# Performance work log

Hardware: AMD Instinct MI355X
Metric: run time of the kernel (lower is better)

Reference implementation:

```python
import jax, jax.numpy as jnp
import numpy as np

EPS = 1e-7
B, C, H, W = 8, 128, 256, 256
HEADS, P = 8, 8
P2 = P * P  # 64
KSIZE = 3


def setup_inputs() -> dict:
    key = jax.random.key(0)
    ks = jax.random.split(key, 9)
    s = 0.05
    x = jax.random.normal(ks[0], (B, C, H, W), jnp.float32)
    Wq = jax.random.normal(ks[1], (P2 * HEADS, P2), jnp.float32) * s
    bq = jax.random.normal(ks[2], (P2 * HEADS,), jnp.float32) * s
    Wk = jax.random.normal(ks[3], (P2 * HEADS, P2), jnp.float32) * s
    bk = jax.random.normal(ks[4], (P2 * HEADS,), jnp.float32) * s
    Wv = jax.random.normal(ks[5], (C, C), jnp.float32) * s  # 1x1 conv squeezed
    bv = jax.random.normal(ks[6], (C,), jnp.float32) * s
    Wp = jax.random.normal(ks[7], (C, 1, KSIZE, KSIZE), jnp.float32) * s  # depthwise
    bp = jax.random.normal(ks[8], (C,), jnp.float32) * s
    return {"x": x, "Wq": Wq, "bq": bq, "Wk": Wk, "bk": bk,
            "Wv": Wv, "bv": bv, "Wp": Wp, "bp": bp}


def _linear_attn(q, k, xv):
    # q, k: [B, heads, C, P2]; xv: [B, heads, C, d2]
    l1, d1 = q.shape[-2], q.shape[-1]
    l2, d2 = xv.shape[-2], xv.shape[-1]
    if l1 * d1 * l2 + l1 * l2 * d2 <= d2 * l2 * d1 + d2 * d1 * l1:
        qk = jnp.einsum('bhcp,bhdp->bhcd', q, k)          # q @ k^T : [B,h,C,C]
        qk = qk / (qk.sum(axis=-1, keepdims=True) + EPS)
        return jnp.einsum('bhcd,bhde->bhce', qk, xv)
    else:
        kx = jnp.einsum('bhcp,bhcd->bhpd', k, xv)          # k^T @ x : [B,h,P2,d2]
        out = jnp.einsum('bhcp,bhpd->bhcd', q, kx)         # q @ (k^T @ x)
        denom = jnp.einsum('bhcp,bhp->bhc', q, k.sum(axis=2)) + EPS  # q @ rowsum(k^T)
        return out / denom[..., None]


def reference(x, Wq, bq, Wk, bk, Wv, bv, Wp, bp):
    Bs, Cs, Hs, Ws = x.shape
    # AdaptiveAvgPool2d(P) with divisible dims == block mean
    pooled = x.reshape(Bs, Cs, P, Hs // P, P, Ws // P).mean(axis=(3, 5))
    pooled = pooled.reshape(Bs, Cs, P2)
    q = jax.nn.relu(pooled @ Wq.T + bq).reshape(Bs, Cs, HEADS, P2).transpose(0, 2, 1, 3)
    k = jax.nn.relu(pooled @ Wk.T + bk).reshape(Bs, Cs, HEADS, P2).transpose(0, 2, 1, 3)
    # 1x1 conv (v)
    v = jnp.einsum('bchw,oc->bohw', x, Wv) + bv[None, :, None, None]
    d2 = (Hs * Ws) // HEADS  # divisible by construction -> no replicate pad
    xv = v.reshape(Bs, Cs, HEADS, d2).transpose(0, 2, 1, 3)
    attn = _linear_attn(q, k, xv)                           # [B,h,C,d2]
    out = attn.transpose(0, 2, 1, 3).reshape(Bs, Cs, Hs, Ws)
    # depthwise 3x3 proj, padding 1
    out = jax.lax.conv_general_dilated(
        out, Wp, window_strides=(1, 1), padding=[(1, 1), (1, 1)],
        dimension_numbers=('NCHW', 'OIHW', 'NCHW'), feature_group_count=Cs)
    return out + bp[None, :, None, None]
```

## Files before the change

kernel.cpp:

```cpp
#include <hip/hip_runtime.h>
#include <hip/hip_bf16.h>

#define HW 65536
#define CCH 128

typedef __attribute__((ext_vector_type(8))) short short8;
typedef __attribute__((ext_vector_type(4))) float f32x4;
typedef __attribute__((ext_vector_type(8))) unsigned short u16x8;

__device__ __forceinline__ void gload_lds16(const void* g, void* l) {
    __builtin_amdgcn_global_load_lds((const __attribute__((address_space(1))) void*)g,
                                     (__attribute__((address_space(3))) void*)l, 16, 0, 0);
}
__device__ __forceinline__ unsigned short f2bf(float f) {
    union { float f; unsigned int i; } u; u.f = f;
    unsigned int r = u.i + 0x7fffu + ((u.i >> 16) & 1u);
    return (unsigned short)(r >> 16);
}
__device__ __forceinline__ float bf2f(unsigned short h) {
    union { unsigned int i; float f; } u; u.i = ((unsigned int)h) << 16; return u.f;
}
__device__ __forceinline__ unsigned int cvt_pk_bf16(float lo, float hi) {
    unsigned int r;
    asm("v_cvt_pk_bf16_f32 %0, %1, %2" : "=v"(r) : "v"(lo), "v"(hi));
    return r;
}
__device__ __forceinline__ void lds_barrier() {
    asm volatile("s_waitcnt lgkmcnt(0)" ::: "memory");
    __builtin_amdgcn_s_barrier();
    __builtin_amdgcn_sched_barrier(0);
}

__global__ __launch_bounds__(256) void pool_kernel(const float* __restrict__ x,
                                                   float* __restrict__ pooled) {
    int bc = blockIdx.x;
    const float* base = x + (size_t)bc * HW;
    int t = threadIdx.x;
    int w = t >> 6, l = t & 63;
    for (int it = 0; it < 2; ++it) {
        int py = w + it * 4;
        const float* rp = base + py * 32 * 256 + l * 4;
        f32x4 s0 = {0.f, 0.f, 0.f, 0.f};
        f32x4 s1 = {0.f, 0.f, 0.f, 0.f};
        #pragma unroll
        for (int r = 0; r < 32; r += 2) {
            s0 += *(const f32x4*)(rp + r * 256);
            s1 += *(const f32x4*)(rp + (r + 1) * 256);
        }
        f32x4 sv = s0 + s1;
        float acc = sv[0] + sv[1] + sv[2] + sv[3];
        acc += __shfl_down(acc, 4, 8);
        acc += __shfl_down(acc, 2, 8);
        acc += __shfl_down(acc, 1, 8);
        if ((l & 7) == 0)
            pooled[(size_t)bc * 64 + py * 8 + (l >> 3)] = acc * (1.0f / 1024.0f);
    }
}

__global__ __launch_bounds__(256) void qkam_kernel(
        const float* __restrict__ pooled,
        const float* __restrict__ Wq, const float* __restrict__ bq,
        const float* __restrict__ Wk, const float* __restrict__ bk,
        const float* __restrict__ bv,
        unsigned short* __restrict__ Ahi, unsigned short* __restrict__ Alo,
        float* __restrict__ beta) {
    int bid = blockIdx.x;
    int bh = bid >> 2;
    int cg = bid & 3;
    int b = bh >> 3, h = bh & 7;
    int t = threadIdx.x;
    __shared__ float ps[128 * 64];
    __shared__ float Wqs[64 * 64];
    __shared__ float Wks[64 * 64];
    __shared__ float ks[128 * 68];
    __shared__ float qs[32 * 68];
    __shared__ float bvs[128];

    for (int i = t; i < 2048; i += 256) {
        int c = i >> 4, p4 = (i & 15) * 4;
        *(f32x4*)&ps[c * 64 + p4] = *(const f32x4*)(pooled + (size_t)(b * CCH + c) * 64 + p4);
    }
    for (int i = t; i < 1024; i += 256) {
        int r = i >> 4, p4 = (i & 15) * 4;
        *(f32x4*)&Wqs[r * 64 + p4] = *(const f32x4*)(Wq + (size_t)(h * 64 + r) * 64 + p4);
        *(f32x4*)&Wks[r * 64 + p4] = *(const f32x4*)(Wk + (size_t)(h * 64 + r) * 64 + p4);
    }
    if (t < 128) bvs[t] = bv[t];
    __syncthreads();

    {
        int p = t & 63, g = t >> 6;
        f32x4 wr[16];
        #pragma unroll
        for (int j = 0; j < 16; ++j) wr[j] = *(const f32x4*)&Wks[p * 64 + j * 4];
        float bkv = bk[h * 64 + p];
        for (int dd = 0; dd < 32; ++dd) {
            int d = g * 32 + dd;
            float acc = bkv;
            #pragma unroll
            for (int j = 0; j < 16; ++j) {
                f32x4 pv = *(const f32x4*)&ps[d * 64 + j * 4];
                acc += pv[0] * wr[j][0] + pv[1] * wr[j][1] + pv[2] * wr[j][2] + pv[3] * wr[j][3];
            }
            ks[d * 68 + p] = fmaxf(acc, 0.f);
        }
        #pragma unroll
        for (int j = 0; j < 16; ++j) wr[j] = *(const f32x4*)&Wqs[p * 64 + j * 4];
        float bqv = bq[h * 64 + p];
        for (int dd = 0; dd < 8; ++dd) {
            int cl = g * 8 + dd;
            int c = cg * 32 + cl;
            float acc = bqv;
            #pragma unroll
            for (int j = 0; j < 16; ++j) {
                f32x4 pv = *(const f32x4*)&ps[c * 64 + j * 4];
                acc += pv[0] * wr[j][0] + pv[1] * wr[j][1] + pv[2] * wr[j][2] + pv[3] * wr[j][3];
            }
            qs[cl * 68 + p] = fmaxf(acc, 0.f);
        }
    }
    __syncthreads();

    {
        int cl = t >> 3, dc = t & 7;
        int c = cg * 32 + cl;
        int d0 = dc * 16;
        f32x4 qr[16];
        #pragma unroll
        for (int ch = 0; ch < 16; ++ch) qr[ch] = *(const f32x4*)&qs[cl * 68 + ch * 4];
        float a[16];
        #pragma unroll
        for (int jr = 0; jr < 16; ++jr) {
            int j = (jr + dc * 2) & 15;
            int d = d0 + j;
            float acc = 0.f;
            #pragma unroll
            for (int ch = 0; ch < 16; ++ch) {
                f32x4 kr = *(const f32x4*)&ks[d * 68 + ch * 4];
                acc += qr[ch][0] * kr[0] + qr[ch][1] * kr[1] + qr[ch][2] * kr[2] + qr[ch][3] * kr[3];
            }
            a[j] = acc;
        }
        float s = 0.f;
        #pragma unroll
        for (int j = 0; j < 16; ++j) s += a[j];
        s += __shfl_xor(s, 1);
        s += __shfl_xor(s, 2);
        s += __shfl_xor(s, 4);
        float inv = 1.0f / (s + 1e-7f);
        float bpart = 0.f;
        union { unsigned short u[16]; uint4 v[2]; } ph, pl;
        #pragma unroll
        for (int j = 0; j < 16; ++j) {
            float an = a[j] * inv;
            bpart += an * bvs[d0 + j];
            unsigned short hi = f2bf(an);
            ph.u[j] = hi;
            pl.u[j] = f2bf(an - bf2f(hi));
        }
        bpart += __shfl_xor(bpart, 1);
        bpart += __shfl_xor(bpart, 2);
        bpart += __shfl_xor(bpart, 4);
        if (dc == 0) beta[bh * 128 + c] = bpart;
        size_t ao = (size_t)bh * 16384 + c * 128 + d0;
        *(uint4*)(Ahi + ao) = ph.v[0];
        *(uint4*)(Ahi + ao + 8) = ph.v[1];
        *(uint4*)(Alo + ao) = pl.v[0];
        *(uint4*)(Alo + ao + 8) = pl.v[1];
    }
}

__global__ __launch_bounds__(256) void am2_kernel(
        const unsigned short* __restrict__ Ahi, const unsigned short* __restrict__ Alo,
        const float* __restrict__ Wv, unsigned short* __restrict__ Mo) {
    int bid = blockIdx.x;
    int bh = bid >> 1;
    int eg = bid & 1;
    int tid = threadIdx.x;
    __shared__ __align__(16) char Wt[65536];
    for (int i = tid; i < 4096; i += 256) {
        int d = i >> 5, e4 = (i & 31) * 4;
        f32x4 v = *(const f32x4*)(Wv + (size_t)d * 128 + e4);
        #pragma unroll
        for (int j = 0; j < 4; ++j) {
            int e = e4 + j;
            unsigned short hi = f2bf(v[j]);
            unsigned short lo = f2bf(v[j] - bf2f(hi));
            int o = (e * 256 + d * 2) ^ ((e & 7) << 4);
            *(unsigned short*)(Wt + o) = hi;
            *(unsigned short*)(Wt + 32768 + o) = lo;
        }
    }
    __syncthreads();
    int w = tid >> 6, l = tid & 63;
    int lc = l & 15, lk = (l >> 4) * 8;
    f32x4 acc[2][4] = {};
    const unsigned short* Ab = Ahi + (size_t)bh * 16384;
    const unsigned short* Alb = Alo + (size_t)bh * 16384;
    #pragma unroll
    for (int ksi = 0; ksi < 4; ++ksi) {
        int d = ksi * 32 + lk;
        short8 ah[2], al[2], bhv[4], blv[4];
        #pragma unroll
        for (int ci = 0; ci < 2; ++ci) {
            int c = w * 32 + ci * 16 + lc;
            ah[ci] = *(const short8*)(Ab + c * 128 + d);
            al[ci] = *(const short8*)(Alb + c * 128 + d);
        }
        #pragma unroll
        for (int ei = 0; ei < 4; ++ei) {
            int e = eg * 64 + ei * 16 + lc;
            int o = (e * 256 + d * 2) ^ ((e & 7) << 4);
            bhv[ei] = *(const short8*)(Wt + o);
            blv[ei] = *(const short8*)(Wt + 32768 + o);
        }
        #pragma unroll
        for (int ci = 0; ci < 2; ++ci)
            #pragma unroll
            for (int ei = 0; ei < 4; ++ei) {
                acc[ci][ei] = __builtin_amdgcn_mfma_f32_16x16x32_bf16(ah[ci], bhv[ei], acc[ci][ei], 0, 0, 0);
                acc[ci][ei] = __builtin_amdgcn_mfma_f32_16x16x32_bf16(ah[ci], blv[ei], acc[ci][ei], 0, 0, 0);
                acc[ci][ei] = __builtin_amdgcn_mfma_f32_16x16x32_bf16(al[ci], bhv[ei], acc[ci][ei], 0, 0, 0);
            }
    }
    unsigned short* Mb = Mo + (size_t)bh * 16384;
    #pragma unroll
    for (int ci = 0; ci < 2; ++ci)
        #pragma unroll
        for (int ei = 0; ei < 4; ++ei)
            #pragma unroll
            for (int r = 0; r < 4; ++r) {
                int c = w * 32 + ci * 16 + (l >> 4) * 4 + r;
                int e = eg * 64 + ei * 16 + lc;
                Mb[c * 128 + e] = f2bf(acc[ci][ei][r]);
            }
}

__global__ __launch_bounds__(512, 4) void attn_kernel(
        const float* __restrict__ x,
        const __hip_bfloat16* __restrict__ Mbf,
        const float* __restrict__ beta,
        __hip_bfloat16* __restrict__ attn) {
    int bid = blockIdx.x;
    int bh = bid >> 3;
    int chunk = bid & 7;
    int b = bh >> 3, h = bh & 7;
    int s0g = h * 8192 + chunk * 1024;
    int tid = threadIdx.x;
    int w = tid >> 6, l = tid & 63;

    __shared__ __align__(16) char sm[81920];
    char* ts0 = sm + 32768;
    char* ost = sm + 65536;

    const char* Mg = (const char*)(Mbf + (size_t)bh * 16384);
    #pragma unroll
    for (int i = 0; i < 4; ++i) {
        int o = i * 8192 + tid * 16;
        int osw = o ^ (((o >> 8) & 15) << 4);
        gload_lds16(Mg + osw, sm + o);
    }

    int e0u = (tid >> 4) * 2;
    int s4u = (tid & 15) * 4;
    const float* xb = x + (size_t)b * CCH * HW + s0g;

    f32x4 rg[4];
    #define LOADT(t_) do { \
        const float* p0 = xb + (size_t)e0u * HW + (t_) * 64 + s4u; \
        rg[0] = *(const f32x4*)p0; \
        rg[1] = *(const f32x4*)(p0 + HW); \
        const float* p1 = p0 + (size_t)64 * HW; \
        rg[2] = *(const f32x4*)p1; \
        rg[3] = *(const f32x4*)(p1 + HW); \
    } while (0)
    #define WRITET(buf_) do { \
        _Pragma("unroll") \
        for (int j = 0; j < 4; ++j) { \
            int s = s4u + j; \
            int sw = (s & 15) << 4; \
            unsigned int pa = cvt_pk_bf16(rg[0][j], rg[1][j]); \
            unsigned int pb = cvt_pk_bf16(rg[2][j], rg[3][j]); \
            *(unsigned int*)((buf_) + ((s * 256 + e0u * 2) ^ sw)) = pa; \
            *(unsigned int*)((buf_) + ((s * 256 + (e0u + 64) * 2) ^ sw)) = pb; \
        } \
    } while (0)

    LOADT(0);
    WRITET(ts0);
    LOADT(1);
    __syncthreads();

    int c0w = (w >> 1) * 32;
    int s0w = (w & 1) * 32;
    short8 mf[2][4];
    #pragma unroll
    for (int ci = 0; ci < 2; ++ci)
        #pragma unroll
        for (int ksi = 0; ksi < 4; ++ksi) {
            int c = c0w + ci * 16 + (l & 15);
            int o = (c * 256 + ksi * 64 + ((l >> 4) * 16)) ^ ((c & 15) << 4);
            mf[ci][ksi] = *(const short8*)(sm + o);
        }
    const float* bet = beta + bh * 128;
    float bv0 = bet[c0w + (l & 15)];
    float bv1 = bet[c0w + 16 + (l & 15)];
    __hip_bfloat16* ab = attn + (size_t)b * CCH * HW + s0g;

    for (int t = 0; t < 16; ++t) {
        char* tsc = ts0 + (t & 1) * 16384;
        if (t < 15) WRITET(ts0 + ((t + 1) & 1) * 16384);
        if (t < 14) LOADT(t + 2);
        f32x4 acc[2][2] = {};
        #pragma unroll
        for (int ksi = 0; ksi < 4; ++ksi) {
            short8 af[2];
            #pragma unroll
            for (int si = 0; si < 2; ++si) {
                int s = s0w + si * 16 + (l & 15);
                int o = (s * 256 + ksi * 64 + ((l >> 4) * 16)) ^ ((s & 15) << 4);
                af[si] = *(const short8*)(tsc + o);
            }
            #pragma unroll
            for (int si = 0; si < 2; ++si)
                #pragma unroll
                for (int ci = 0; ci < 2; ++ci)
                    acc[si][ci] = __builtin_amdgcn_mfma_f32_16x16x32_bf16(af[si], mf[ci][ksi], acc[si][ci], 0, 0, 0);
        }
        #pragma unroll
        for (int si = 0; si < 2; ++si)
            #pragma unroll
            for (int ci = 0; ci < 2; ++ci) {
                int sb = s0w + si * 16 + (l >> 4) * 4;
                int c = c0w + ci * 16 + (l & 15);
                float bvv = ci ? bv1 : bv0;
                uint2 pk2;
                pk2.x = cvt_pk_bf16(acc[si][ci][0] + bvv, acc[si][ci][1] + bvv);
                pk2.y = cvt_pk_bf16(acc[si][ci][2] + bvv, acc[si][ci][3] + bvv);
                int o = (c * 128 + sb * 2) ^ ((c & 7) << 4);
                *(uint2*)(ost + o) = pk2;
            }
        lds_barrier();
        #pragma unroll
        for (int p = 0; p < 2; ++p) {
            int c = p * 64 + (tid >> 3);
            int kk = tid & 7;
            int o = (c * 128 + kk * 16) ^ ((c & 7) << 4);
            *(int4*)((char*)(ab + (size_t)c * HW + t * 64) + kk * 16) = *(const int4*)(ost + o);
        }
        lds_barrier();
    }
    #undef LOADT
    #undef WRITET
}

__global__ __launch_bounds__(256) void dwconv_kernel(const __hip_bfloat16* __restrict__ attn,
        const float* __restrict__ Wp, const float* __restrict__ bp,
        float* __restrict__ out) {
    int bid = blockIdx.x;
    int bc = bid >> 3;
    int ys = bid & 7;
    int y0 = ys * 32;
    int t = threadIdx.x;
    __shared__ unsigned short tile[34][264];
    const unsigned short* base = (const unsigned short*)attn + (size_t)bc * HW;
    for (int i = t; i < 34 * 32; i += 256) {
        int r = i >> 5, ck = i & 31;
        int gy = y0 + r - 1;
        u16x8 v;
        if (gy >= 0 && gy < 256) v = *(const u16x8*)(base + gy * 256 + ck * 8);
        else v = (u16x8)((unsigned short)0);
        *(u16x8*)&tile[r][ck * 8] = v;
    }
    __syncthreads();
    int c = bc & 127;
    float wv[9];
    #pragma unroll
    for (int j = 0; j < 9; ++j) wv[j] = Wp[c * 9 + j];
    float bias = bp[c];
    float* obase = out + (size_t)bc * HW;
    for (int p = 0; p < 4; ++p) {
        int orow = p * 8 + (t >> 5);
        int oc = (t & 31) * 8;
        float accv[8];
        #pragma unroll
        for (int j = 0; j < 8; ++j) accv[j] = bias;
        #pragma unroll
        for (int dy = 0; dy < 3; ++dy) {
            int tr = orow + dy;
            u16x8 m = *(const u16x8*)&tile[tr][oc];
            float f[10];
            f[0] = (oc == 0) ? 0.f : bf2f(tile[tr][oc - 1]);
            #pragma unroll
            for (int j = 0; j < 8; ++j) f[j + 1] = bf2f(m[j]);
            f[9] = (oc == 248) ? 0.f : bf2f(tile[tr][oc + 8]);
            float w0 = wv[dy * 3], w1 = wv[dy * 3 + 1], w2 = wv[dy * 3 + 2];
            #pragma unroll
            for (int j = 0; j < 8; ++j)
                accv[j] += w0 * f[j] + w1 * f[j + 1] + w2 * f[j + 2];
        }
        float* op = obase + (size_t)(y0 + orow) * 256 + oc;
        float4 o0 = {accv[0], accv[1], accv[2], accv[3]};
        float4 o1 = {accv[4], accv[5], accv[6], accv[7]};
        *(float4*)op = o0;
        *(float4*)(op + 4) = o1;
    }
}

extern "C" void kernel_launch(void* const* d_in, const int* in_sizes, int n_in,
                              void* d_out, int out_size, void* d_ws, size_t ws_size,
                              hipStream_t stream) {
    const float* x  = (const float*)d_in[0];
    const float* Wq = (const float*)d_in[1];
    const float* bq = (const float*)d_in[2];
    const float* Wk = (const float*)d_in[3];
    const float* bk = (const float*)d_in[4];
    const float* Wv = (const float*)d_in[5];
    const float* bv = (const float*)d_in[6];
    const float* Wp = (const float*)d_in[7];
    const float* bp = (const float*)d_in[8];
    float* out = (float*)d_out;
    char* ws = (char*)d_ws;

    float* pooled      = (float*)ws;
    unsigned short* Ahi = (unsigned short*)(ws + 262144);
    unsigned short* Alo = (unsigned short*)(ws + 2359296);
    unsigned short* Mo  = (unsigned short*)(ws + 4456448);
    float* betab       = (float*)(ws + 6553600);
    char* attnp        = ws + 6586368;

    pool_kernel<<<dim3(1024), dim3(256), 0, stream>>>(x, pooled);
    qkam_kernel<<<dim3(256), dim3(256), 0, stream>>>(pooled, Wq, bq, Wk, bk, bv, Ahi, Alo, betab);
    am2_kernel<<<dim3(128), dim3(256), 0, stream>>>(Ahi, Alo, Wv, Mo);
    attn_kernel<<<dim3(512), dim3(512), 0, stream>>>(x, (const __hip_bfloat16*)Mo, betab, (__hip_bfloat16*)attnp);
    dwconv_kernel<<<dim3(8192), dim3(256), 0, stream>>>((const __hip_bfloat16*)attnp, Wp, bp, out);
}
```

Baseline: 266.4 us.

## Rebalance attn kernel work over 768 blocks and shrink LDS for higher occupancy

The attention GEMM kernel now splits each (batch, head) into 12 blocks of 10–11 tiles instead of 8 blocks of 16 tiles, launching 768 blocks to fill the GPU's 256 CUs more evenly. LDS use drops from 80KB to 48KB by reusing the M staging area for the x tile double buffer once the M fragments are in registers, and launch bounds rise to 6 waves-per-EU to allow more resident blocks. The cost is an extra barrier, uneven per-block work (10 vs 11 tiles), and possibly more register pressure under the tighter launch bound.

```diff
diff --git a/kernel.cpp b/kernel.cpp
--- a/kernel.cpp
+++ b/kernel.cpp
@@ -236,38 +236,30 @@
             }
 }
 
-__global__ __launch_bounds__(512, 4) void attn_kernel(
+__global__ __launch_bounds__(512, 6) void attn_kernel(
         const float* __restrict__ x,
         const __hip_bfloat16* __restrict__ Mbf,
         const float* __restrict__ beta,
         __hip_bfloat16* __restrict__ attn) {
     int bid = blockIdx.x;
-    int bh = bid >> 3;
-    int chunk = bid & 7;
+    int bh = bid / 12;
+    int r12 = bid % 12;
     int b = bh >> 3, h = bh & 7;
-    int s0g = h * 8192 + chunk * 1024;
+    int start = (r12 < 8) ? r12 * 11 : 88 + (r12 - 8) * 10;
+    int ntile = (r12 < 8) ? 11 : 10;
     int tid = threadIdx.x;
     int w = tid >> 6, l = tid & 63;
 
-    __shared__ __align__(16) char sm[81920];
-    char* ts0 = sm + 32768;
-    char* ost = sm + 65536;
-
-    const char* Mg = (const char*)(Mbf + (size_t)bh * 16384);
-    #pragma unroll
-    for (int i = 0; i < 4; ++i) {
-        int o = i * 8192 + tid * 16;
-        int osw = o ^ (((o >> 8) & 15) << 4);
-        gload_lds16(Mg + osw, sm + o);
-    }
+    __shared__ __align__(16) char sm[49152];
+    char* ost = sm + 32768;
 
     int e0u = (tid >> 4) * 2;
     int s4u = (tid & 15) * 4;
-    const float* xb = x + (size_t)b * CCH * HW + s0g;
+    const float* xb = x + (size_t)b * CCH * HW + h * 8192;
 
     f32x4 rg[4];
-    #define LOADT(t_) do { \
-        const float* p0 = xb + (size_t)e0u * HW + (t_) * 64 + s4u; \
+    #define LOADT(T_) do { \
+        const float* p0 = xb + (size_t)e0u * HW + (T_) * 64 + s4u; \
         rg[0] = *(const f32x4*)p0; \
         rg[1] = *(const f32x4*)(p0 + HW); \
         const float* p1 = p0 + (size_t)64 * HW; \
@@ -286,9 +278,14 @@
         } \
     } while (0)
 
-    LOADT(0);
-    WRITET(ts0);
-    LOADT(1);
+    LOADT(start);
+    const char* Mg = (const char*)(Mbf + (size_t)bh * 16384);
+    #pragma unroll
+    for (int i = 0; i < 4; ++i) {
+        int o = i * 8192 + tid * 16;
+        int osw = o ^ (((o >> 8) & 15) << 4);
+        gload_lds16(Mg + osw, sm + o);
+    }
     __syncthreads();
 
     int c0w = (w >> 1) * 32;
@@ -305,12 +302,17 @@
     const float* bet = beta + bh * 128;
     float bv0 = bet[c0w + (l & 15)];
     float bv1 = bet[c0w + 16 + (l & 15)];
-    __hip_bfloat16* ab = attn + (size_t)b * CCH * HW + s0g;
-
-    for (int t = 0; t < 16; ++t) {
-        char* tsc = ts0 + (t & 1) * 16384;
-        if (t < 15) WRITET(ts0 + ((t + 1) & 1) * 16384);
-        if (t < 14) LOADT(t + 2);
+    __hip_bfloat16* ab = attn + (size_t)b * CCH * HW + h * 8192;
+    lds_barrier();
+
+    WRITET(sm);
+    LOADT(start + 1);
+    lds_barrier();
+
+    for (int t = 0; t < ntile; ++t) {
+        char* tsc = sm + (t & 1) * 16384;
+        if (t + 1 < ntile) WRITET(sm + ((t + 1) & 1) * 16384);
+        if (t + 2 < ntile) LOADT(start + t + 2);
         f32x4 acc[2][2] = {};
         #pragma unroll
         for (int ksi = 0; ksi < 4; ++ksi) {
@@ -341,12 +343,13 @@
                 *(uint2*)(ost + o) = pk2;
             }
         lds_barrier();
+        int T = start + t;
         #pragma unroll
         for (int p = 0; p < 2; ++p) {
             int c = p * 64 + (tid >> 3);
             int kk = tid & 7;
             int o = (c * 128 + kk * 16) ^ ((c & 7) << 4);
-            *(int4*)((char*)(ab + (size_t)c * HW + t * 64) + kk * 16) = *(const int4*)(ost + o);
+            *(int4*)((char*)(ab + (size_t)c * HW + T * 64) + kk * 16) = *(const int4*)(ost + o);
         }
         lds_barrier();
     }
@@ -432,6 +435,6 @@
     pool_kernel<<<dim3(1024), dim3(256), 0, stream>>>(x, pooled);
     qkam_kernel<<<dim3(256), dim3(256), 0, stream>>>(pooled, Wq, bq, Wk, bk, bv, Ahi, Alo, betab);
     am2_kernel<<<dim3(128), dim3(256), 0, stream>>>(Ahi, Alo, Wv, Mo);
-    attn_kernel<<<dim3(512), dim3(512), 0, stream>>>(x, (const __hip_bfloat16*)Mo, betab, (__hip_bfloat16*)attnp);
+    attn_kernel<<<dim3(768), dim3(512), 0, stream>>>(x, (const __hip_bfloat16*)Mo, betab, (__hip_bfloat16*)attnp);
     dwconv_kernel<<<dim3(8192), dim3(256), 0, stream>>>((const __hip_bfloat16*)attnp, Wp, bp, out);
 }
```

Result: slower. 272.7 us (+2.3%).
